# Optimization experiments

Measured on AMD Instinct MI355X. Metric: run time of the kernel, lower is better.

## Reference

```python
import jax, jax.numpy as jnp
import numpy as np

D = 1024
H = 16
HD = D // H
S = 2048
B = 2
INNER = 4 * D
EPS = 1e-5


def _layernorm(x, w, b):
    mu = jnp.mean(x, axis=-1, keepdims=True)
    var = jnp.mean(jnp.square(x - mu), axis=-1, keepdims=True)
    return (x - mu) * jax.lax.rsqrt(var + EPS) * w + b


def _rope(x, cos, sin):
    # x: [B, S, H, HD]; cos/sin: [S, HD//2]
    xe, xo = x[..., 0::2], x[..., 1::2]
    c = cos[None, :, None, :]
    s = sin[None, :, None, :]
    oe = xe * c - xo * s
    oo = xe * s + xo * c
    return jnp.stack([oe, oo], axis=-1).reshape(x.shape)


def setup_inputs() -> dict:
    key = jax.random.key(0)
    ks = jax.random.split(key, 12)
    hidden_states = jax.random.normal(ks[0], (B, S, D), dtype=jnp.float32)
    time_step_emb = jax.random.normal(ks[1], (B, 6 * D), dtype=jnp.float32)
    # causal additive mask [1,1,S,S]
    causal = jnp.tril(jnp.ones((S, S), dtype=bool))
    attention_mask = jnp.where(causal, 0.0, -1e9).astype(jnp.float32)[None, None]
    # proper RoPE tables
    inv_freq = 1.0 / (10000.0 ** (np.arange(0, HD, 2, dtype=np.float32) / HD))
    t = np.arange(S, dtype=np.float32)
    freqs = np.outer(t, inv_freq)  # [S, HD//2]
    rope_cos = jnp.asarray(np.cos(freqs))
    rope_sin = jnp.asarray(np.sin(freqs))
    p = 0.02
    params = dict(
        ln1_w=jnp.ones((D,), jnp.float32), ln1_b=jnp.zeros((D,), jnp.float32),
        ln2_w=jnp.ones((D,), jnp.float32), ln2_b=jnp.zeros((D,), jnp.float32),
        c_attn_w=jax.random.normal(ks[2], (D, 3 * D), jnp.float32) * p,
        c_attn_b=jnp.zeros((3 * D,), jnp.float32),
        c_proj_w=jax.random.normal(ks[3], (D, D), jnp.float32) * p,
        c_proj_b=jnp.zeros((D,), jnp.float32),
        fc_w=jax.random.normal(ks[4], (D, INNER), jnp.float32) * p,
        fc_b=jnp.zeros((INNER,), jnp.float32),
        proj_w=jax.random.normal(ks[5], (INNER, D), jnp.float32) * p,
        proj_b=jnp.zeros((D,), jnp.float32),
        scale_shift_table=jax.random.normal(ks[6], (6, D), jnp.float32) / np.sqrt(D),
    )
    return dict(hidden_states=hidden_states, attention_mask=attention_mask,
                time_step_emb=time_step_emb, rope_cos=rope_cos, rope_sin=rope_sin,
                **params)


def reference(hidden_states, attention_mask, time_step_emb, rope_cos, rope_sin,
              ln1_w, ln1_b, ln2_w, ln2_b, c_attn_w, c_attn_b, c_proj_w, c_proj_b,
              fc_w, fc_b, proj_w, proj_b, scale_shift_table):
    b = hidden_states.shape[0]
    mods = scale_shift_table[None] + time_step_emb.reshape(b, 6, D)  # [B,6,D]
    sh_msa, sc_msa, g_msa, sh_mlp, sc_mlp, g_mlp = [mods[:, i:i + 1] for i in range(6)]

    residual = hidden_states
    h = _layernorm(hidden_states, ln1_w, ln1_b) * (1.0 + sc_msa) + sh_msa

    qkv = h @ c_attn_w + c_attn_b  # [B,S,3D]
    q, k, v = jnp.split(qkv, 3, axis=-1)
    q = _rope(q.reshape(b, S, H, HD), rope_cos, rope_sin)
    k = _rope(k.reshape(b, S, H, HD), rope_cos, rope_sin)
    v = v.reshape(b, S, H, HD)
    scores = jnp.einsum('bqhd,bkhd->bhqk', q, k) / np.sqrt(float(HD))
    scores = scores + attention_mask
    attn = jax.nn.softmax(scores, axis=-1)
    out = jnp.einsum('bhqk,bkhd->bqhd', attn, v).reshape(b, S, D)
    attn_out = out @ c_proj_w + c_proj_b

    hidden = attn_out * g_msa + residual
    residual = hidden
    h = _layernorm(hidden, ln2_w, ln2_b) * (1.0 + sc_mlp) + sh_mlp
    h = jax.nn.gelu(h @ fc_w + fc_b, approximate=True)  # gelu_new (tanh approx)
    h = h @ proj_w + proj_b
    return h * g_mlp + residual
```

## Files before the change

### kernel.cpp

```cpp
#include <hip/hip_runtime.h>
#include <hip/hip_bf16.h>

#define D_MODEL 1024
#define N_HEADS 16
#define HEAD_DIM 64
#define SEQ 2048
#define BATCH 2
#define INNER_DIM 4096
#define ROWS (BATCH*SEQ)

using f32x4  = __attribute__((ext_vector_type(4))) float;
using bf16x8 = __attribute__((ext_vector_type(8))) short;

__device__ __forceinline__ void gl_lds16(const void* g, void* l) {
  __builtin_amdgcn_global_load_lds(
      (const __attribute__((address_space(1))) void*)g,
      (__attribute__((address_space(3))) void*)l, 16, 0, 0);
}

__device__ __forceinline__ float bf2f(unsigned short u) {
  union { unsigned int i; float f; } v; v.i = ((unsigned int)u) << 16; return v.f;
}
__device__ __forceinline__ unsigned short f2bf(float f) {
  union { float f; unsigned int i; } v; v.f = f;
  unsigned int x = v.i;
  return (unsigned short)((x + 0x7fffu + ((x >> 16) & 1u)) >> 16);
}

__device__ __forceinline__ float exp2fast(float x) {
  return __builtin_amdgcn_exp2f(x);
}

__device__ __forceinline__ float gelu_tanh(float x) {
  float x3 = x * x * x;
  float z = 0.7978845608028654f * (x + 0.044715f * x3);
  z = fminf(z, 15.0f);
  float e = __expf(2.0f * z);
  float th = (e - 1.0f) / (e + 1.0f);
  return 0.5f * x * (1.0f + th);
}

__global__ void transpose_convert(const float* __restrict__ in,
                                  unsigned short* __restrict__ out,
                                  int K, int N) {
  __shared__ float tile[32][33];
  int n0 = blockIdx.x * 32, k0 = blockIdx.y * 32;
  int tx = threadIdx.x, ty = threadIdx.y;
#pragma unroll
  for (int i = 0; i < 4; i++)
    tile[ty + i * 8][tx] = in[(size_t)(k0 + ty + i * 8) * N + n0 + tx];
  __syncthreads();
#pragma unroll
  for (int i = 0; i < 4; i++)
    out[(size_t)(n0 + ty + i * 8) * K + k0 + tx] = f2bf(tile[tx][ty + i * 8]);
}

template<int SH_IDX, int SC_IDX>
__global__ void ln_mod_kernel(const float* __restrict__ x,
                              const float* __restrict__ lw,
                              const float* __restrict__ lb,
                              const float* __restrict__ sst,
                              const float* __restrict__ temb,
                              unsigned short* __restrict__ out) {
  int row = blockIdx.x;
  int b = row >> 11;
  int t = threadIdx.x;
  const float* xr = x + (size_t)row * D_MODEL;
  float4 v = ((const float4*)xr)[t];
  float s = v.x + v.y + v.z + v.w;
  float s2 = v.x * v.x + v.y * v.y + v.z * v.z + v.w * v.w;
#pragma unroll
  for (int o = 1; o < 64; o <<= 1) { s += __shfl_xor(s, o); s2 += __shfl_xor(s2, o); }
  __shared__ float red[8];
  int wid = t >> 6, lane = t & 63;
  if (lane == 0) { red[wid] = s; red[4 + wid] = s2; }
  __syncthreads();
  s = red[0] + red[1] + red[2] + red[3];
  s2 = red[4] + red[5] + red[6] + red[7];
  float mu = s * (1.0f / D_MODEL);
  float var = s2 * (1.0f / D_MODEL) - mu * mu;
  float rs = rsqrtf(var + 1e-5f);
  int d0 = t * 4;
  float xv[4] = { v.x, v.y, v.z, v.w };
  ushort4 ov;
  unsigned short* po = (unsigned short*)&ov;
#pragma unroll
  for (int j = 0; j < 4; j++) {
    int d = d0 + j;
    float ln = (xv[j] - mu) * rs * lw[d] + lb[d];
    float sc = sst[SC_IDX * D_MODEL + d] + temb[b * 6 * D_MODEL + SC_IDX * D_MODEL + d];
    float sh = sst[SH_IDX * D_MODEL + d] + temb[b * 6 * D_MODEL + SH_IDX * D_MODEL + d];
    po[j] = f2bf(ln * (1.0f + sc) + sh);
  }
  *((ushort4*)(out + (size_t)row * D_MODEL + d0)) = ov;
}

__global__ void rope_kernel(unsigned short* __restrict__ qkv,
                            const float* __restrict__ cosb,
                            const float* __restrict__ sinb) {
  int t = blockIdx.x * blockDim.x + threadIdx.x;
  int row = t >> 10;
  int rem = t & 1023;
  int qk = rem >> 9;
  int rem2 = rem & 511;
  int hh = rem2 >> 5;
  int i = rem2 & 31;
  int s = row & (SEQ - 1);
  unsigned int* p = (unsigned int*)(qkv + (size_t)row * 3072 + qk * 1024 + hh * 64 + 2 * i);
  unsigned int pv = *p;
  float xe = bf2f((unsigned short)(pv & 0xffff));
  float xo = bf2f((unsigned short)(pv >> 16));
  float c = cosb[s * 32 + i], sn = sinb[s * 32 + i];
  float sc = (qk == 0) ? 0.18033688011112042f : 1.0f;
  float oe = (xe * c - xo * sn) * sc;
  float oo = (xe * sn + xo * c) * sc;
  *p = (((unsigned int)f2bf(oo)) << 16) | (unsigned int)f2bf(oe);
}

enum { EPI_BF16 = 0, EPI_RES = 1, EPI_GELU = 2, EPI_FINAL = 3 };

template<int EPI, int BMF>
__global__ __launch_bounds__(256, 2)
void gemm_kernel(const unsigned short* __restrict__ A,
                 const unsigned short* __restrict__ Bt,
                 const float* __restrict__ bias,
                 void* __restrict__ Cout,
                 int N, int K,
                 const float* __restrict__ sst,
                 const float* __restrict__ temb,
                 int g_idx,
                 const float* __restrict__ res) {
  __shared__ unsigned short Alds[2][BMF * 32 * 32];
  __shared__ unsigned short Blds[2][128 * 32];
  const int t = threadIdx.x;
  const int w = t >> 6, l = t & 63;
  const int lg = l >> 4, ll = l & 15;
  const int wm = w >> 1, wn = w & 1;

  const int nx = gridDim.x;
  const int nwg = nx * gridDim.y;
  const int lid = blockIdx.y * nx + blockIdx.x;
  const int nid = (lid & 7) * (nwg >> 3) + (lid >> 3);
  const int m0 = (nid / nx) * (BMF * 32), n0 = (nid % nx) * 128;

  f32x4 acc[BMF][4] = {};

  auto stage = [&](int k0, int buf) {
#pragma unroll
    for (int i = 0; i < BMF / 2; i++) {
      int c = i * 256 + t;
      int row = c >> 2, ch = c & 3;
      int chs = ch ^ ((row >> 1) & 3);
      gl_lds16(A + (size_t)(m0 + row) * K + k0 + chs * 8, (char*)&Alds[buf][0] + c * 16);
    }
#pragma unroll
    for (int i = 0; i < 2; i++) {
      int c = i * 256 + t;
      int row = c >> 2, ch = c & 3;
      int chs = ch ^ ((row >> 1) & 3);
      gl_lds16(Bt + (size_t)(n0 + row) * K + k0 + chs * 8, (char*)&Blds[buf][0] + c * 16);
    }
  };

  stage(0, 0);
  int buf = 0;
  for (int k0 = 0; k0 < K; k0 += 32) {
    const bool hn = (k0 + 32 < K);
    if (hn) {
      stage(k0 + 32, buf ^ 1);
      if constexpr (BMF == 4) asm volatile("s_waitcnt vmcnt(4)" ::: "memory");
      else                    asm volatile("s_waitcnt vmcnt(3)" ::: "memory");
    } else {
      asm volatile("s_waitcnt vmcnt(0)" ::: "memory");
    }
    __builtin_amdgcn_s_barrier();
    asm volatile("" ::: "memory");

    bf16x8 af[BMF], bfr[4];
#pragma unroll
    for (int mf = 0; mf < BMF; mf++) {
      int row = wm * (BMF * 16) + mf * 16 + ll;
      int ch = lg ^ ((row >> 1) & 3);
      af[mf] = *(const bf16x8*)((const char*)&Alds[buf][0] + row * 64 + ch * 16);
    }
#pragma unroll
    for (int nf = 0; nf < 4; nf++) {
      int row = wn * 64 + nf * 16 + ll;
      int ch = lg ^ ((row >> 1) & 3);
      bfr[nf] = *(const bf16x8*)((const char*)&Blds[buf][0] + row * 64 + ch * 16);
    }
#pragma unroll
    for (int mf = 0; mf < BMF; mf++)
#pragma unroll
      for (int nf = 0; nf < 4; nf++)
        acc[mf][nf] = __builtin_amdgcn_mfma_f32_16x16x32_bf16(af[mf], bfr[nf], acc[mf][nf], 0, 0, 0);

    asm volatile("" ::: "memory");
    __builtin_amdgcn_s_barrier();
    buf ^= 1;
  }

#pragma unroll
  for (int mf = 0; mf < BMF; mf++) {
#pragma unroll
    for (int nf = 0; nf < 4; nf++) {
      int col = n0 + wn * 64 + nf * 16 + ll;
      float bv = bias[col];
#pragma unroll
      for (int r = 0; r < 4; r++) {
        int row = m0 + wm * (BMF * 16) + mf * 16 + lg * 4 + r;
        float v = acc[mf][nf][r] + bv;
        if constexpr (EPI == EPI_BF16) {
          ((unsigned short*)Cout)[(size_t)row * N + col] = f2bf(v);
        } else if constexpr (EPI == EPI_GELU) {
          ((unsigned short*)Cout)[(size_t)row * N + col] = f2bf(gelu_tanh(v));
        } else {
          int bb = row >> 11;
          float g = sst[g_idx * D_MODEL + col] + temb[bb * 6 * D_MODEL + g_idx * D_MODEL + col];
          ((float*)Cout)[(size_t)row * N + col] = v * g + res[(size_t)row * N + col];
        }
      }
    }
  }
}

__global__ __launch_bounds__(256, 4)
void attn_kernel(const unsigned short* __restrict__ qkv,
                 unsigned short* __restrict__ attn_o) {
  __shared__ unsigned short Klds[2][64 * 64];
  __shared__ unsigned short Vt[2][64 * 64];
  __shared__ unsigned short Plds[4][16 * 64];

  const int id = blockIdx.x;
  const int bh = id & 31;
  const int b = bh >> 4, h = bh & 15;
  const int q0 = (id >> 5) * 64;
  const int t = threadIdx.x;
  const int w = t >> 6, l = t & 63;
  const int lg = l >> 4, ll = l & 15;
  const int qw0 = q0 + w * 16;
  const int q_lane = qw0 + ll;

  bf16x8 qf[2];
  {
    const unsigned short* qb = qkv + (size_t)(b * SEQ + q_lane) * 3072 + h * 64;
    qf[0] = *(const bf16x8*)(qb + lg * 8);
    qf[1] = *(const bf16x8*)(qb + 32 + lg * 8);
  }

  const int kp = t & 31, dg = t >> 5;

  f32x4 oacc[4] = {};
  float mrun = -1e30f, lrun = 0.0f;

  {
#pragma unroll
    for (int i = 0; i < 2; i++) {
      int c = i * 256 + t;
      int kr = c >> 3, cc = c & 7;
      gl_lds16(qkv + (size_t)(b * SEQ + kr) * 3072 + 1024 + h * 64 + (cc ^ (kr & 7)) * 8,
               (char*)&Klds[0][0] + c * 16);
    }
    const unsigned short* vp = qkv + (size_t)(b * SEQ + 2 * kp) * 3072 + 2048 + h * 64 + dg * 8;
    union { uint4 u; unsigned short s[8]; } a0, a1;
    a0.u = *(const uint4*)vp;
    a1.u = *(const uint4*)(vp + 3072);
    unsigned int* vt32 = (unsigned int*)&Vt[0][0];
#pragma unroll
    for (int i = 0; i < 8; i++)
      vt32[(dg * 8 + i) * 32 + (((kp >> 2) ^ i) << 2) + (kp & 3)] =
          (unsigned int)a0.s[i] | ((unsigned int)a1.s[i] << 16);
  }
  __syncthreads();

  int buf = 0;
  for (int k0 = 0; k0 <= q0; k0 += 64) {
    const bool has_next = (k0 + 64 <= q0);
    union { uint4 u; unsigned short s[8]; } n0, n1;
    if (has_next) {
#pragma unroll
      for (int i = 0; i < 2; i++) {
        int c = i * 256 + t;
        int kr = c >> 3, cc = c & 7;
        gl_lds16(qkv + (size_t)(b * SEQ + k0 + 64 + kr) * 3072 + 1024 + h * 64 + (cc ^ (kr & 7)) * 8,
                 (char*)&Klds[buf ^ 1][0] + c * 16);
      }
      const unsigned short* vp =
          qkv + (size_t)(b * SEQ + k0 + 64 + 2 * kp) * 3072 + 2048 + h * 64 + dg * 8;
      n0.u = *(const uint4*)vp;
      n1.u = *(const uint4*)(vp + 3072);
    }

    f32x4 s[4] = {};
#pragma unroll
    for (int kk = 0; kk < 2; kk++) {
#pragma unroll
      for (int nf = 0; nf < 4; nf++) {
        int key = nf * 16 + ll;
        int cc = (kk * 4 + lg) ^ (key & 7);
        bf16x8 kf = *(const bf16x8*)((const char*)&Klds[buf][0] + key * 128 + cc * 16);
        s[nf] = __builtin_amdgcn_mfma_f32_16x16x32_bf16(kf, qf[kk], s[nf], 0, 0, 0);
      }
    }
    if (k0 == q0) {
#pragma unroll
      for (int nf = 0; nf < 4; nf++) {
        int key = k0 + nf * 16 + lg * 4;
#pragma unroll
        for (int r = 0; r < 4; r++)
          if (key + r > q_lane) s[nf][r] = -1e30f;
      }
    }
    float mx = -1e30f;
#pragma unroll
    for (int nf = 0; nf < 4; nf++)
#pragma unroll
      for (int r = 0; r < 4; r++) mx = fmaxf(mx, s[nf][r]);
    mx = fmaxf(mx, __shfl_xor(mx, 16));
    mx = fmaxf(mx, __shfl_xor(mx, 32));
    float mnew = fmaxf(mrun, mx);
    float alpha = exp2fast(mrun - mnew);
    mrun = mnew;
    float ps = 0.0f;
#pragma unroll
    for (int nf = 0; nf < 4; nf++)
#pragma unroll
      for (int r = 0; r < 4; r++) {
        float p = exp2fast(s[nf][r] - mnew);
        s[nf][r] = p;
        ps += p;
      }
    ps += __shfl_xor(ps, 16);
    ps += __shfl_xor(ps, 32);
    lrun = lrun * alpha + ps;
#pragma unroll
    for (int nf = 0; nf < 4; nf++)
#pragma unroll
      for (int r = 0; r < 4; r++) oacc[nf][r] *= alpha;

#pragma unroll
    for (int nf = 0; nf < 4; nf++) {
      unsigned int lo = (unsigned int)f2bf(s[nf][0]) | ((unsigned int)f2bf(s[nf][1]) << 16);
      unsigned int hi = (unsigned int)f2bf(s[nf][2]) | ((unsigned int)f2bf(s[nf][3]) << 16);
      int chunk = (nf * 2 + (lg >> 1)) ^ (ll & 7);
      uint2 pv; pv.x = lo; pv.y = hi;
      *(uint2*)((char*)&Plds[w][0] + ll * 128 + chunk * 16 + (lg & 1) * 8) = pv;
    }
    bf16x8 pb[2];
#pragma unroll
    for (int kk = 0; kk < 2; kk++) {
      int pc = (kk * 4 + lg) ^ (ll & 7);
      pb[kk] = *(const bf16x8*)((char*)&Plds[w][0] + ll * 128 + pc * 16);
    }
#pragma unroll
    for (int nf = 0; nf < 4; nf++) {
      int d = nf * 16 + ll;
#pragma unroll
      for (int kk = 0; kk < 2; kk++) {
        int vc = (kk * 4 + lg) ^ (d & 7);
        bf16x8 vb = *(const bf16x8*)((const char*)&Vt[buf][0] + d * 128 + vc * 16);
        oacc[nf] = __builtin_amdgcn_mfma_f32_16x16x32_bf16(vb, pb[kk], oacc[nf], 0, 0, 0);
      }
    }
    if (has_next) {
      unsigned int* vt32 = (unsigned int*)&Vt[buf ^ 1][0];
#pragma unroll
      for (int i = 0; i < 8; i++)
        vt32[(dg * 8 + i) * 32 + (((kp >> 2) ^ i) << 2) + (kp & 3)] =
            (unsigned int)n0.s[i] | ((unsigned int)n1.s[i] << 16);
    }
    __syncthreads();
    buf ^= 1;
  }

  float rl = 1.0f / lrun;
#pragma unroll
  for (int nf = 0; nf < 4; nf++) {
    ushort4 ov;
    ov.x = f2bf(oacc[nf][0] * rl);
    ov.y = f2bf(oacc[nf][1] * rl);
    ov.z = f2bf(oacc[nf][2] * rl);
    ov.w = f2bf(oacc[nf][3] * rl);
    *(ushort4*)(attn_o + (size_t)(b * SEQ + q_lane) * D_MODEL + h * 64 + nf * 16 + lg * 4) = ov;
  }
}

extern "C" void kernel_launch(void* const* d_in, const int* in_sizes, int n_in,
                              void* d_out, int out_size, void* d_ws, size_t ws_size,
                              hipStream_t stream) {
  const float* hidden_states = (const float*)d_in[0];
  const float* temb     = (const float*)d_in[2];
  const float* rope_cos = (const float*)d_in[3];
  const float* rope_sin = (const float*)d_in[4];
  const float* ln1_w    = (const float*)d_in[5];
  const float* ln1_b    = (const float*)d_in[6];
  const float* ln2_w    = (const float*)d_in[7];
  const float* ln2_b    = (const float*)d_in[8];
  const float* c_attn_w = (const float*)d_in[9];
  const float* c_attn_b = (const float*)d_in[10];
  const float* c_proj_w = (const float*)d_in[11];
  const float* c_proj_b = (const float*)d_in[12];
  const float* fc_w     = (const float*)d_in[13];
  const float* fc_b     = (const float*)d_in[14];
  const float* proj_w   = (const float*)d_in[15];
  const float* proj_b   = (const float*)d_in[16];
  const float* sst      = (const float*)d_in[17];

  char* ws = (char*)d_ws;
  unsigned short* wqkv  = (unsigned short*)(ws + 0);
  unsigned short* wproj = (unsigned short*)(ws + 6291456);
  unsigned short* wfc   = (unsigned short*)(ws + 8388608);
  unsigned short* wp2   = (unsigned short*)(ws + 16777216);
  unsigned short* hln   = (unsigned short*)(ws + 25165824);
  unsigned short* qkvb  = (unsigned short*)(ws + 33554432);
  unsigned short* attno = (unsigned short*)(ws + 58720256);
  unsigned short* h3    = (unsigned short*)(ws + 33554432);
  float*          hidden = (float*)(ws + 67108864);

  dim3 tb(32, 8);
  transpose_convert<<<dim3(3072 / 32, 1024 / 32), tb, 0, stream>>>(c_attn_w, wqkv, 1024, 3072);
  transpose_convert<<<dim3(1024 / 32, 1024 / 32), tb, 0, stream>>>(c_proj_w, wproj, 1024, 1024);
  transpose_convert<<<dim3(4096 / 32, 1024 / 32), tb, 0, stream>>>(fc_w, wfc, 1024, 4096);
  transpose_convert<<<dim3(1024 / 32, 4096 / 32), tb, 0, stream>>>(proj_w, wp2, 4096, 1024);

  ln_mod_kernel<0, 1><<<ROWS, 256, 0, stream>>>(hidden_states, ln1_w, ln1_b, sst, temb, hln);

  gemm_kernel<EPI_BF16, 4><<<dim3(3072 / 128, ROWS / 128), 256, 0, stream>>>(
      hln, wqkv, c_attn_b, qkvb, 3072, 1024, nullptr, nullptr, 0, nullptr);

  rope_kernel<<<(ROWS * 1024) / 256, 256, 0, stream>>>(qkvb, rope_cos, rope_sin);

  attn_kernel<<<dim3(32 * 32), 256, 0, stream>>>(qkvb, attno);

  gemm_kernel<EPI_RES, 2><<<dim3(1024 / 128, ROWS / 64), 256, 0, stream>>>(
      attno, wproj, c_proj_b, hidden, 1024, 1024, sst, temb, 2, hidden_states);

  ln_mod_kernel<3, 4><<<ROWS, 256, 0, stream>>>(hidden, ln2_w, ln2_b, sst, temb, hln);

  gemm_kernel<EPI_GELU, 4><<<dim3(4096 / 128, ROWS / 128), 256, 0, stream>>>(
      hln, wfc, fc_b, h3, 4096, 1024, nullptr, nullptr, 0, nullptr);

  gemm_kernel<EPI_FINAL, 2><<<dim3(1024 / 128, ROWS / 64), 256, 0, stream>>>(
      h3, wp2, proj_b, d_out, 1024, 4096, sst, temb, 5, hidden);
}
```

Baseline: 283.8 us.

## Fuse RoPE into QKV GEMM epilogue and deepen GEMM LDS pipeline to four stages

Removes the separate rope_kernel. RoPE and the Q scaling are now applied in the QKV GEMM epilogue, with a lane shuffle that pairs the even and odd columns. This saves a full read-modify-write pass over the QKV buffer and one launch. Separately, the GEMM main loop moves from double buffering to a 4-deep LDS ring with three tiles prefetched and matching vmcnt waits, to hide more global-load latency. The cost is doubled LDS per block, which may lower occupancy under launch_bounds(256,2).

```diff
diff --git a/kernel.cpp b/kernel.cpp
--- a/kernel.cpp
+++ b/kernel.cpp
@@ -95,29 +95,7 @@
   *((ushort4*)(out + (size_t)row * D_MODEL + d0)) = ov;
 }
 
-__global__ void rope_kernel(unsigned short* __restrict__ qkv,
-                            const float* __restrict__ cosb,
-                            const float* __restrict__ sinb) {
-  int t = blockIdx.x * blockDim.x + threadIdx.x;
-  int row = t >> 10;
-  int rem = t & 1023;
-  int qk = rem >> 9;
-  int rem2 = rem & 511;
-  int hh = rem2 >> 5;
-  int i = rem2 & 31;
-  int s = row & (SEQ - 1);
-  unsigned int* p = (unsigned int*)(qkv + (size_t)row * 3072 + qk * 1024 + hh * 64 + 2 * i);
-  unsigned int pv = *p;
-  float xe = bf2f((unsigned short)(pv & 0xffff));
-  float xo = bf2f((unsigned short)(pv >> 16));
-  float c = cosb[s * 32 + i], sn = sinb[s * 32 + i];
-  float sc = (qk == 0) ? 0.18033688011112042f : 1.0f;
-  float oe = (xe * c - xo * sn) * sc;
-  float oo = (xe * sn + xo * c) * sc;
-  *p = (((unsigned int)f2bf(oo)) << 16) | (unsigned int)f2bf(oe);
-}
-
-enum { EPI_BF16 = 0, EPI_RES = 1, EPI_GELU = 2, EPI_FINAL = 3 };
+enum { EPI_QKV = 0, EPI_RES = 1, EPI_GELU = 2, EPI_FINAL = 3 };
 
 template<int EPI, int BMF>
 __global__ __launch_bounds__(256, 2)
@@ -129,9 +107,12 @@
                  const float* __restrict__ sst,
                  const float* __restrict__ temb,
                  int g_idx,
-                 const float* __restrict__ res) {
-  __shared__ unsigned short Alds[2][BMF * 32 * 32];
-  __shared__ unsigned short Blds[2][128 * 32];
+                 const float* __restrict__ res,
+                 const float* __restrict__ cosb,
+                 const float* __restrict__ sinb) {
+  constexpr int NBUF = 4;
+  __shared__ unsigned short Alds[NBUF][BMF * 32 * 32];
+  __shared__ unsigned short Blds[NBUF][128 * 32];
   const int t = threadIdx.x;
   const int w = t >> 6, l = t & 63;
   const int lg = l >> 4, ll = l & 15;
@@ -162,20 +143,8 @@
     }
   };
 
-  stage(0, 0);
-  int buf = 0;
-  for (int k0 = 0; k0 < K; k0 += 32) {
-    const bool hn = (k0 + 32 < K);
-    if (hn) {
-      stage(k0 + 32, buf ^ 1);
-      if constexpr (BMF == 4) asm volatile("s_waitcnt vmcnt(4)" ::: "memory");
-      else                    asm volatile("s_waitcnt vmcnt(3)" ::: "memory");
-    } else {
-      asm volatile("s_waitcnt vmcnt(0)" ::: "memory");
-    }
-    __builtin_amdgcn_s_barrier();
+  auto comp = [&](int buf) {
     asm volatile("" ::: "memory");
-
     bf16x8 af[BMF], bfr[4];
 #pragma unroll
     for (int mf = 0; mf < BMF; mf++) {
@@ -194,11 +163,28 @@
 #pragma unroll
       for (int nf = 0; nf < 4; nf++)
         acc[mf][nf] = __builtin_amdgcn_mfma_f32_16x16x32_bf16(af[mf], bfr[nf], acc[mf][nf], 0, 0, 0);
-
     asm volatile("" ::: "memory");
+  };
+
+  const int nk = K >> 5;
+  stage(0, 0); stage(32, 1); stage(64, 2);
+  int it = 0;
+  for (; it + 3 < nk; ++it) {
+    stage((it + 3) * 32, (it + 3) & 3);
+    if constexpr (BMF == 4) asm volatile("s_waitcnt vmcnt(12)" ::: "memory");
+    else                    asm volatile("s_waitcnt vmcnt(9)" ::: "memory");
     __builtin_amdgcn_s_barrier();
-    buf ^= 1;
-  }
+    comp(it & 3);
+    __builtin_amdgcn_s_barrier();
+  }
+  if constexpr (BMF == 4) asm volatile("s_waitcnt vmcnt(8)" ::: "memory");
+  else                    asm volatile("s_waitcnt vmcnt(6)" ::: "memory");
+  __builtin_amdgcn_s_barrier(); comp(it & 3); __builtin_amdgcn_s_barrier(); ++it;
+  if constexpr (BMF == 4) asm volatile("s_waitcnt vmcnt(4)" ::: "memory");
+  else                    asm volatile("s_waitcnt vmcnt(3)" ::: "memory");
+  __builtin_amdgcn_s_barrier(); comp(it & 3); __builtin_amdgcn_s_barrier(); ++it;
+  asm volatile("s_waitcnt vmcnt(0)" ::: "memory");
+  __builtin_amdgcn_s_barrier(); comp(it & 3); __builtin_amdgcn_s_barrier();
 
 #pragma unroll
   for (int mf = 0; mf < BMF; mf++) {
@@ -210,7 +196,16 @@
       for (int r = 0; r < 4; r++) {
         int row = m0 + wm * (BMF * 16) + mf * 16 + lg * 4 + r;
         float v = acc[mf][nf][r] + bv;
-        if constexpr (EPI == EPI_BF16) {
+        if constexpr (EPI == EPI_QKV) {
+          if (col < 2048) {
+            float vp = __shfl_xor(v, 1);
+            int sp = row & (SEQ - 1);
+            int ip = (col & 63) >> 1;
+            float cz = cosb[sp * 32 + ip], sz = sinb[sp * 32 + ip];
+            float ov = (col & 1) ? (vp * sz + v * cz) : (v * cz - vp * sz);
+            if (col < 1024) ov *= 0.18033688011112042f;
+            v = ov;
+          }
           ((unsigned short*)Cout)[(size_t)row * N + col] = f2bf(v);
         } else if constexpr (EPI == EPI_GELU) {
           ((unsigned short*)Cout)[(size_t)row * N + col] = f2bf(gelu_tanh(v));
@@ -425,21 +420,19 @@
 
   ln_mod_kernel<0, 1><<<ROWS, 256, 0, stream>>>(hidden_states, ln1_w, ln1_b, sst, temb, hln);
 
-  gemm_kernel<EPI_BF16, 4><<<dim3(3072 / 128, ROWS / 128), 256, 0, stream>>>(
-      hln, wqkv, c_attn_b, qkvb, 3072, 1024, nullptr, nullptr, 0, nullptr);
-
-  rope_kernel<<<(ROWS * 1024) / 256, 256, 0, stream>>>(qkvb, rope_cos, rope_sin);
+  gemm_kernel<EPI_QKV, 4><<<dim3(3072 / 128, ROWS / 128), 256, 0, stream>>>(
+      hln, wqkv, c_attn_b, qkvb, 3072, 1024, nullptr, nullptr, 0, nullptr, rope_cos, rope_sin);
 
   attn_kernel<<<dim3(32 * 32), 256, 0, stream>>>(qkvb, attno);
 
   gemm_kernel<EPI_RES, 2><<<dim3(1024 / 128, ROWS / 64), 256, 0, stream>>>(
-      attno, wproj, c_proj_b, hidden, 1024, 1024, sst, temb, 2, hidden_states);
+      attno, wproj, c_proj_b, hidden, 1024, 1024, sst, temb, 2, hidden_states, nullptr, nullptr);
 
   ln_mod_kernel<3, 4><<<ROWS, 256, 0, stream>>>(hidden, ln2_w, ln2_b, sst, temb, hln);
 
   gemm_kernel<EPI_GELU, 4><<<dim3(4096 / 128, ROWS / 128), 256, 0, stream>>>(
-      hln, wfc, fc_b, h3, 4096, 1024, nullptr, nullptr, 0, nullptr);
+      hln, wfc, fc_b, h3, 4096, 1024, nullptr, nullptr, 0, nullptr, nullptr, nullptr);
 
   gemm_kernel<EPI_FINAL, 2><<<dim3(1024 / 128, ROWS / 64), 256, 0, stream>>>(
-      h3, wp2, proj_b, d_out, 1024, 4096, sst, temb, 5, hidden);
-}
+      h3, wp2, proj_b, d_out, 1024, 4096, sst, temb, 5, hidden, nullptr, nullptr);
+}
```

Measured after the change: 301.6 us. 1.06x slower.
